# Kernel optimization log

Hardware: AMD Instinct MI355X
Metric: run time of the kernel (lower is better)

Reference implementation:

```python
import jax, jax.numpy as jnp
import numpy as np

N = 4096        # nodes
IN_FEATS = 256
N_HIDDEN = 128
N_CLASSES = 32
E = 131072      # edges for the GAE blocks (avg degree 32)
TEMP = 0.2
ALPHA = 1.0
EPS = 1e-6
CHUNK = 64      # row-chunk size for masked max aggregation


def _glorot(key, shape):
    fan = shape[0] + shape[1]
    return jax.random.normal(key, shape, jnp.float32) * jnp.sqrt(2.0 / fan)


def setup_inputs():
    key = jax.random.key(0)
    ks = jax.random.split(key, 20)
    return {
        'adj': jax.random.uniform(ks[0], (N, N), jnp.float32),
        'inputs': jax.random.normal(ks[1], (N, IN_FEATS), jnp.float32),
        'feat_inputs': jax.random.normal(ks[2], (N, IN_FEATS), jnp.float32),
        'u': jax.random.uniform(ks[3], (N, N), jnp.float32),
        'src': jax.random.randint(ks[4], (E,), 0, N, jnp.int32),
        'dst': jax.random.randint(ks[5], (E,), 0, N, jnp.int32),
        # GAE GraphConv params (in->hidden, hidden->hidden)
        'gc0_W': _glorot(ks[6], (IN_FEATS, N_HIDDEN)), 'gc0_b': jnp.zeros((N_HIDDEN,), jnp.float32),
        'gc1_W': _glorot(ks[7], (N_HIDDEN, N_HIDDEN)), 'gc1_b': jnp.zeros((N_HIDDEN,), jnp.float32),
        # GraphSAGE layer 0 (in -> hidden), maxpool aggregator
        'p0_W': _glorot(ks[8], (IN_FEATS, IN_FEATS)), 'p0_b': jnp.zeros((IN_FEATS,), jnp.float32),
        'l0_W': _glorot(ks[9], (IN_FEATS, N_HIDDEN)), 'l0_b': jnp.zeros((N_HIDDEN,), jnp.float32),
        'b0': jnp.zeros((N_HIDDEN,), jnp.float32),
        # GraphSAGE layer 1 (hidden -> hidden)
        'p1_W': _glorot(ks[10], (N_HIDDEN, N_HIDDEN)), 'p1_b': jnp.zeros((N_HIDDEN,), jnp.float32),
        'l1_W': _glorot(ks[11], (N_HIDDEN, N_HIDDEN)), 'l1_b': jnp.zeros((N_HIDDEN,), jnp.float32),
        'b1': jnp.zeros((N_HIDDEN,), jnp.float32),
        # GraphSAGE layer 2 (hidden -> classes)
        'p2_W': _glorot(ks[12], (N_HIDDEN, N_HIDDEN)), 'p2_b': jnp.zeros((N_HIDDEN,), jnp.float32),
        'l2_W': _glorot(ks[13], (N_HIDDEN, N_CLASSES)), 'l2_b': jnp.zeros((N_CLASSES,), jnp.float32),
        'b2': jnp.zeros((N_CLASSES,), jnp.float32),
    }


def _graph_conv(h, W, b, src, dst, out_norm, in_norm):
    # DGL GraphConv, norm='both': D_in^{-1/2} A D_out^{-1/2} X W + b
    h = h @ W
    h = h * out_norm[:, None]
    agg = jax.ops.segment_sum(h[src], dst, num_segments=N)
    return agg * in_norm[:, None] + b


def _masked_max(mask, z):
    # h_new[i] = max_{j: mask[i, j]} z[j]; chunk over destination rows to bound memory
    n, d = z.shape
    m = mask.reshape(n // CHUNK, CHUNK, n)
    def body(carry, mc):
        out = jnp.max(jnp.where(mc[:, :, None], z[None, :, :], -jnp.inf), axis=1)
        return carry, out
    _, outs = jax.lax.scan(body, None, m)
    return outs.reshape(n, d)


def _l2norm(x):
    return x / jnp.maximum(jnp.linalg.norm(x, axis=1, keepdims=True), 1e-12)


def _forward(adj, inputs, feat_inputs, u, src, dst,
             gc0_W, gc0_b, gc1_W, gc1_b,
             p0_W, p0_b, l0_W, l0_b, b0,
             p1_W, p1_b, l1_W, l1_b, b1,
             p2_W, p2_b, l2_W, l2_b, b2):
    ones = jnp.ones((E,), jnp.float32)
    out_norm = jnp.maximum(jax.ops.segment_sum(ones, src, num_segments=N), 1.0) ** -0.5
    in_norm = jnp.maximum(jax.ops.segment_sum(ones, dst, num_segments=N), 1.0) ** -0.5
    # --- GAE encode (dropout inactive at inference) ---
    h = jax.nn.relu(_graph_conv(inputs, gc0_W, gc0_b, src, dst, out_norm, in_norm))
    h = _graph_conv(h, gc1_W, gc1_b, src, dst, out_norm, in_norm)
    # --- GAE decode ---
    ep = jax.nn.sigmoid(h @ h.T)
    # --- interpolate ---
    P = ALPHA * (ep / jnp.max(ep)) + (1.0 - ALPHA) * adj
    # --- RelaxedBernoulli straight-through sampling ---
    Pc = jnp.clip(P, EPS, 1.0 - EPS)
    uc = jnp.clip(u, EPS, 1.0 - EPS)
    logits = jnp.log(Pc) - jnp.log1p(-Pc)
    noise = jnp.log(uc) - jnp.log1p(-uc)        # logistic noise
    soft = jax.nn.sigmoid((logits + noise) / TEMP)
    y = soft + jax.lax.stop_gradient(jnp.round(soft) - soft)
    yt = jnp.triu(y, 1)
    A = yt + yt.T
    # --- normalize_adj: diag=1, L1 row normalize; original detaches here ---
    eye = jnp.eye(N, dtype=bool)
    A = jnp.where(eye, 1.0, A)
    A = A / jnp.maximum(jnp.sum(A, axis=1, keepdims=True), 1e-12)
    A = jax.lax.stop_gradient(A)
    mask = A != 0.0   # symmetric graph structure incl. self-loops
    # --- GraphSAGE with maxpool aggregator (dropout inactive) ---
    h = feat_inputs
    layers = ((p0_W, p0_b, l0_W, l0_b, b0, False),
              (p1_W, p1_b, l1_W, l1_b, b1, False),
              (p2_W, p2_b, l2_W, l2_b, b2, True))
    for pW, pb, lW, lb, bb, last in layers:
        z = jax.nn.relu(h @ pW + pb)
        agg = _masked_max(mask, z)
        h = agg @ lW + lb + bb
        if not last:
            h = _l2norm(jax.nn.relu(h))
    return h


def reference(adj, inputs, feat_inputs, u, src, dst,
              gc0_W, gc0_b, gc1_W, gc1_b,
              p0_W, p0_b, l0_W, l0_b, b0,
              p1_W, p1_b, l1_W, l1_b, b1,
              p2_W, p2_b, l2_W, l2_b, b2):
    return _forward(adj, inputs, feat_inputs, u, src, dst,
                    gc0_W, gc0_b, gc1_W, gc1_b,
                    p0_W, p0_b, l0_W, l0_b, b0,
                    p1_W, p1_b, l1_W, l1_b, b1,
                    p2_W, p2_b, l2_W, l2_b, b2)
```

## Files before the change

kernel.cpp:

```cpp
#include <hip/hip_runtime.h>
#include <hip/hip_fp16.h>
#include <cstdint>
#include <cstddef>

#define NN 4096
#define EE 131072
#define TS 64

__device__ __forceinline__ unsigned fkey(float f) {
    unsigned u = __float_as_uint(f);
    return (u & 0x80000000u) ? ~u : (u | 0x80000000u);
}
__device__ __forceinline__ float funkey(unsigned k) {
    unsigned u = (k & 0x80000000u) ? (k & 0x7fffffffu) : ~k;
    return __uint_as_float(u);
}

__device__ __forceinline__ void pkmax(unsigned& a, unsigned x) {
    asm("v_pk_max_f16 %0, %0, %1" : "+v"(a) : "v"(x));
}
__device__ __forceinline__ unsigned bit_sext_s(unsigned w, int off) {
    return (unsigned)(((int)(w << (31 - off))) >> 31);
}

__global__ void k_count(const int* __restrict__ src, const int* __restrict__ dst,
                        int* __restrict__ cs, int* __restrict__ cd) {
    int e = blockIdx.x * 256 + threadIdx.x;
    if (e < EE) {
        atomicAdd(&cs[src[e]], 1);
        atomicAdd(&cd[dst[e]], 1);
    }
}

__global__ void k_norm(const int* __restrict__ cs, const int* __restrict__ cd,
                       float* __restrict__ on, float* __restrict__ inn) {
    int i = blockIdx.x * 256 + threadIdx.x;
    if (i < NN) {
        int a = cs[i] > 1 ? cs[i] : 1;
        int b = cd[i] > 1 ? cd[i] : 1;
        on[i]  = 1.0f / sqrtf((float)a);
        inn[i] = 1.0f / sqrtf((float)b);
    }
}

template<int K, int ND, int RB>
__global__ void k_gemm_scale(const float* __restrict__ X, const float* __restrict__ W,
                             const float* __restrict__ scale, float* __restrict__ out) {
    __shared__ float xr[RB][K];
    int i0 = blockIdx.x * RB;
    for (int t = threadIdx.x; t < RB * K; t += ND)
        xr[t / K][t % K] = X[(size_t)(i0 + t / K) * K + t % K];
    __syncthreads();
    int j = threadIdx.x;
    float acc[RB];
    #pragma unroll
    for (int r = 0; r < RB; ++r) acc[r] = 0.0f;
    #pragma unroll 4
    for (int k = 0; k < K; ++k) {
        float w = W[k * ND + j];
        #pragma unroll
        for (int r = 0; r < RB; ++r) acc[r] = fmaf(xr[r][k], w, acc[r]);
    }
    #pragma unroll
    for (int r = 0; r < RB; ++r)
        out[(size_t)(i0 + r) * ND + j] = acc[r] * scale[i0 + r];
}

template<int K, int ND, int RB, int H16>
__global__ void k_gemm_ab(const float* __restrict__ X, const float* __restrict__ W,
                          const float* __restrict__ b1, float* __restrict__ out) {
    __shared__ float xr[RB][K];
    int i0 = blockIdx.x * RB;
    for (int t = threadIdx.x; t < RB * K; t += ND)
        xr[t / K][t % K] = X[(size_t)(i0 + t / K) * K + t % K];
    __syncthreads();
    int j = threadIdx.x;
    float acc[RB];
    #pragma unroll
    for (int r = 0; r < RB; ++r) acc[r] = 0.0f;
    #pragma unroll 4
    for (int k = 0; k < K; ++k) {
        float w = W[k * ND + j];
        #pragma unroll
        for (int r = 0; r < RB; ++r) acc[r] = fmaf(xr[r][k], w, acc[r]);
    }
    if constexpr (H16) {
        unsigned* oh = (unsigned*)out;
        #pragma unroll
        for (int r = 0; r < RB; ++r) {
            float v = fmaxf(acc[r] + b1[j], 0.0f);
            float o2 = __shfl_xor(v, 1, 64);
            if ((j & 1) == 0) {
                __half2 h = __floats2half2_rn(v, o2);
                oh[(size_t)(i0 + r) * (ND / 2) + (j >> 1)] = *(unsigned*)&h;
            }
        }
    } else {
        #pragma unroll
        for (int r = 0; r < RB; ++r)
            out[(size_t)(i0 + r) * ND + j] = acc[r] + b1[j];
    }
}

template<int K, int ND, int NS, int RB, int L2N>
__global__ void k_gemm_mrgh(const unsigned* __restrict__ Xh, size_t xstride,
                            const float* __restrict__ W,
                            const float* __restrict__ b1, const float* __restrict__ b2,
                            float* __restrict__ out) {
    __shared__ float xr[RB][K];
    int i0 = blockIdx.x * RB;
    for (int t = threadIdx.x; t < RB * (K / 2); t += ND) {
        int r = t / (K / 2), c = t % (K / 2);
        size_t off = (size_t)(i0 + r) * (K / 2) + c;
        unsigned v = Xh[off];
        #pragma unroll
        for (int s = 1; s < NS; ++s) pkmax(v, Xh[(size_t)s * xstride + off]);
        __half2 h = *(__half2*)&v;
        float2 f = __half22float2(h);
        xr[r][2 * c] = f.x;
        xr[r][2 * c + 1] = f.y;
    }
    __syncthreads();
    int j = threadIdx.x;
    float acc[RB];
    #pragma unroll
    for (int r = 0; r < RB; ++r) acc[r] = 0.0f;
    #pragma unroll 4
    for (int k = 0; k < K; ++k) {
        float w = W[k * ND + j];
        #pragma unroll
        for (int r = 0; r < RB; ++r) acc[r] = fmaf(xr[r][k], w, acc[r]);
    }
    if constexpr (L2N) {
        float v[RB], ss[RB];
        #pragma unroll
        for (int r = 0; r < RB; ++r) {
            float t = acc[r] + b1[j];
            if (b2) t += b2[j];
            v[r] = fmaxf(t, 0.0f);
            ss[r] = v[r] * v[r];
        }
        #pragma unroll
        for (int o = 1; o < 64; o <<= 1)
            #pragma unroll
            for (int r = 0; r < RB; ++r) ss[r] += __shfl_xor(ss[r], o, 64);
        __shared__ float sred[RB][2];
        if ((threadIdx.x & 63) == 0)
            #pragma unroll
            for (int r = 0; r < RB; ++r) sred[r][threadIdx.x >> 6] = ss[r];
        __syncthreads();
        #pragma unroll
        for (int r = 0; r < RB; ++r) {
            float tot = sred[r][0] + sred[r][1];
            out[(size_t)(i0 + r) * ND + j] = v[r] / fmaxf(sqrtf(tot), 1e-12f);
        }
    } else {
        #pragma unroll
        for (int r = 0; r < RB; ++r) {
            float v = acc[r] + b1[j];
            if (b2) v += b2[j];
            out[(size_t)(i0 + r) * ND + j] = v;
        }
    }
}

__global__ void k_scatter(const float* __restrict__ t, const int* __restrict__ src,
                          const int* __restrict__ dst, float* __restrict__ agg) {
    int e = blockIdx.x;
    int j = threadIdx.x;
    int s = src[e], d = dst[e];
    atomicAdd(&agg[(size_t)d * 128 + j], t[(size_t)s * 128 + j]);
}

__global__ void k_gcn_out(const float* __restrict__ agg, const float* __restrict__ inn,
                          const float* __restrict__ b, float* __restrict__ out, int do_relu) {
    int idx = blockIdx.x * 256 + threadIdx.x;
    int i = idx >> 7, j = idx & 127;
    float v = agg[idx] * inn[i] + b[j];
    if (do_relu) v = fmaxf(v, 0.0f);
    out[idx] = v;
}

template<int MODE>
__global__ __launch_bounds__(256, 4) void k_stile(const float* __restrict__ h,
                                                  const float* __restrict__ u,
                                                  unsigned* __restrict__ smax_key,
                                                  unsigned* __restrict__ mb) {
    int ti = blockIdx.y, tj = blockIdx.x;
    if (tj < ti) return;
    __shared__ float Ah[TS][68];
    __shared__ float Bh[TS][68];
    int tid = threadIdx.x;
    int tx = tid & 15, ty = tid >> 4;
    const float* ha = h + (size_t)ti * TS * 128;
    const float* hb = h + (size_t)tj * TS * 128;

    float acc[4][4];
    #pragma unroll
    for (int r = 0; r < 4; ++r)
        #pragma unroll
        for (int c = 0; c < 4; ++c) acc[r][c] = 0.0f;

    for (int half = 0; half < 2; ++half) {
        __syncthreads();
        #pragma unroll
        for (int t = 0; t < 4; ++t) {
            int f = tid + t * 256;
            int row = f >> 4, kk = f & 15;
            *(float4*)&Ah[row][kk * 4] = *(const float4*)(ha + (size_t)row * 128 + half * 64 + kk * 4);
            *(float4*)&Bh[row][kk * 4] = *(const float4*)(hb + (size_t)row * 128 + half * 64 + kk * 4);
        }
        __syncthreads();
        #pragma unroll 2
        for (int k4 = 0; k4 < 16; ++k4) {
            float4 a[4], b[4];
            #pragma unroll
            for (int r = 0; r < 4; ++r) a[r] = *(const float4*)&Ah[ty + 16 * r][k4 * 4];
            #pragma unroll
            for (int c = 0; c < 4; ++c) b[c] = *(const float4*)&Bh[tx + 16 * c][k4 * 4];
            #pragma unroll
            for (int r = 0; r < 4; ++r)
                #pragma unroll
                for (int c = 0; c < 4; ++c) {
                    acc[r][c] = fmaf(a[r].x, b[c].x, acc[r][c]);
                    acc[r][c] = fmaf(a[r].y, b[c].y, acc[r][c]);
                    acc[r][c] = fmaf(a[r].z, b[c].z, acc[r][c]);
                    acc[r][c] = fmaf(a[r].w, b[c].w, acc[r][c]);
                }
        }
    }

    if constexpr (MODE == 0) {
        float m = -3.4e38f;
        #pragma unroll
        for (int r = 0; r < 4; ++r)
            #pragma unroll
            for (int c = 0; c < 4; ++c) m = fmaxf(m, acc[r][c]);
        #pragma unroll
        for (int o = 1; o < 64; o <<= 1) m = fmaxf(m, __shfl_xor(m, o, 64));
        __shared__ float wm[4];
        if ((tid & 63) == 0) wm[tid >> 6] = m;
        __syncthreads();
        if (tid == 0) {
            float mm = fmaxf(fmaxf(wm[0], wm[1]), fmaxf(wm[2], wm[3]));
            atomicMax(smax_key, fkey(mm));
        }
    } else {
        float smax = funkey(*smax_key);
        float epmax = 1.0f / (1.0f + expf(-smax));
        __shared__ unsigned lm[TS][2];
        __shared__ unsigned lmT[TS][2];
        if (tid < 128) { lm[tid >> 1][tid & 1] = 0u; lmT[tid >> 1][tid & 1] = 0u; }
        __syncthreads();
        #pragma unroll
        for (int r = 0; r < 4; ++r) {
            #pragma unroll
            for (int c = 0; c < 4; ++c) {
                int li = ty + 16 * r, lj = tx + 16 * c;
                int gi = ti * TS + li, gj = tj * TS + lj;
                bool bit = false;
                if (gi < gj) {
                    float ep = 1.0f / (1.0f + expf(-acc[r][c]));
                    float P = ep / epmax;
                    float Pc = fminf(fmaxf(P, 1e-6f), 1.0f - 1e-6f);
                    float uu = u[(size_t)gi * NN + gj];
                    float ucv = fminf(fmaxf(uu, 1e-6f), 1.0f - 1e-6f);
                    bit = Pc > (1.0f - ucv);
                } else if (gi == gj) {
                    bit = true;
                }
                if (bit) {
                    atomicOr(&lm[li][lj >> 5], 1u << (lj & 31));
                    atomicOr(&lmT[lj][li >> 5], 1u << (li & 31));
                }
            }
        }
        __syncthreads();
        if (tid < 128) {
            int r = tid >> 1, wq = tid & 1;
            unsigned word = lm[r][wq];
            if (ti == tj) word |= lmT[r][wq];
            mb[(size_t)(ti * TS + r) * 128 + tj * 2 + wq] = word;
        } else if (ti != tj) {
            int r = (tid - 128) >> 1, wq = tid & 1;
            mb[(size_t)(tj * TS + r) * 128 + ti * 2 + wq] = lmT[r][wq];
        }
    }
}

__global__ __launch_bounds__(256, 4) void k_stile_store(const float* __restrict__ h,
                                                        float* __restrict__ S,
                                                        unsigned* __restrict__ smax_key) {
    int ti = blockIdx.y, tj = blockIdx.x;
    if (tj < ti) return;
    __shared__ float Ah[TS][68];
    __shared__ float Bh[TS][68];
    int tid = threadIdx.x;
    int tx = tid & 15, ty = tid >> 4;
    const float* ha = h + (size_t)ti * TS * 128;
    const float* hb = h + (size_t)tj * TS * 128;

    float acc[4][4];
    #pragma unroll
    for (int r = 0; r < 4; ++r)
        #pragma unroll
        for (int c = 0; c < 4; ++c) acc[r][c] = 0.0f;

    for (int half = 0; half < 2; ++half) {
        __syncthreads();
        #pragma unroll
        for (int t = 0; t < 4; ++t) {
            int f = tid + t * 256;
            int row = f >> 4, kk = f & 15;
            *(float4*)&Ah[row][kk * 4] = *(const float4*)(ha + (size_t)row * 128 + half * 64 + kk * 4);
            *(float4*)&Bh[row][kk * 4] = *(const float4*)(hb + (size_t)row * 128 + half * 64 + kk * 4);
        }
        __syncthreads();
        #pragma unroll 2
        for (int k4 = 0; k4 < 16; ++k4) {
            float4 a[4], b[4];
            #pragma unroll
            for (int r = 0; r < 4; ++r) a[r] = *(const float4*)&Ah[ty + 16 * r][k4 * 4];
            #pragma unroll
            for (int c = 0; c < 4; ++c) b[c] = *(const float4*)&Bh[tx + 16 * c][k4 * 4];
            #pragma unroll
            for (int r = 0; r < 4; ++r)
                #pragma unroll
                for (int c = 0; c < 4; ++c) {
                    acc[r][c] = fmaf(a[r].x, b[c].x, acc[r][c]);
                    acc[r][c] = fmaf(a[r].y, b[c].y, acc[r][c]);
                    acc[r][c] = fmaf(a[r].z, b[c].z, acc[r][c]);
                    acc[r][c] = fmaf(a[r].w, b[c].w, acc[r][c]);
                }
        }
    }

    float* sp = S + (size_t)(ti * 64 + tj) * 4096;
    #pragma unroll
    for (int r = 0; r < 4; ++r)
        #pragma unroll
        for (int c = 0; c < 4; ++c)
            sp[(ty + 16 * r) * 64 + tx + 16 * c] = acc[r][c];

    float m = -3.4e38f;
    #pragma unroll
    for (int r = 0; r < 4; ++r)
        #pragma unroll
        for (int c = 0; c < 4; ++c) m = fmaxf(m, acc[r][c]);
    #pragma unroll
    for (int o = 1; o < 64; o <<= 1) m = fmaxf(m, __shfl_xor(m, o, 64));
    __shared__ float wm[4];
    if ((tid & 63) == 0) wm[tid >> 6] = m;
    __syncthreads();
    if (tid == 0)
        atomicMax(smax_key, fkey(fmaxf(fmaxf(wm[0], wm[1]), fmaxf(wm[2], wm[3]))));
}

__global__ __launch_bounds__(256, 4) void k_bitemit(const float* __restrict__ S,
                                                    const float* __restrict__ u,
                                                    const unsigned* __restrict__ smax_key,
                                                    unsigned* __restrict__ mb) {
    int ti = blockIdx.y, tj = blockIdx.x;
    if (tj < ti) return;
    int tid = threadIdx.x;
    int tx = tid & 15, ty = tid >> 4;
    float smax = funkey(*smax_key);
    float epmax = 1.0f / (1.0f + expf(-smax));
    __shared__ unsigned lm[TS][2];
    __shared__ unsigned lmT[TS][2];
    if (tid < 128) { lm[tid >> 1][tid & 1] = 0u; lmT[tid >> 1][tid & 1] = 0u; }
    __syncthreads();
    const float* sp = S + (size_t)(ti * 64 + tj) * 4096;
    #pragma unroll
    for (int r = 0; r < 4; ++r) {
        #pragma unroll
        for (int c = 0; c < 4; ++c) {
            int li = ty + 16 * r, lj = tx + 16 * c;
            int gi = ti * TS + li, gj = tj * TS + lj;
            bool bit = false;
            if (gi < gj) {
                float ep = 1.0f / (1.0f + expf(-sp[li * 64 + lj]));
                float P = ep / epmax;
                float Pc = fminf(fmaxf(P, 1e-6f), 1.0f - 1e-6f);
                float uu = u[(size_t)gi * NN + gj];
                float ucv = fminf(fmaxf(uu, 1e-6f), 1.0f - 1e-6f);
                bit = Pc > (1.0f - ucv);
            } else if (gi == gj) {
                bit = true;
            }
            if (bit) {
                atomicOr(&lm[li][lj >> 5], 1u << (lj & 31));
                atomicOr(&lmT[lj][li >> 5], 1u << (li & 31));
            }
        }
    }
    __syncthreads();
    if (tid < 128) {
        int r = tid >> 1, wq = tid & 1;
        unsigned word = lm[r][wq];
        if (ti == tj) word |= lmT[r][wq];
        mb[(size_t)(ti * TS + r) * 128 + tj * 2 + wq] = word;
    } else if (ti != tj) {
        int r = (tid - 128) >> 1, wq = tid & 1;
        mb[(size_t)(tj * TS + r) * 128 + ti * 2 + wq] = lmT[r][wq];
    }
}

template<int RT, int JS>
__global__ __launch_bounds__(256, 8) void k_mmax256h(const unsigned* __restrict__ mb,
                                                     const unsigned* __restrict__ zh,
                                                     unsigned* __restrict__ pmh) {
    constexpr int JPS = NN / JS;
    constexpr int WPS = JPS / 32;
    constexpr int RPG = RT / 4;
    constexpr int NRB = NN / RT;
    int rowblk = blockIdx.x % NRB, js = blockIdx.x / NRB;
    int i0 = rowblk * RT;

    __shared__ unsigned msk[RT][WPS + 1];
    {
        int t = threadIdx.x;
        msk[t / WPS][t % WPS] = mb[(size_t)(i0 + t / WPS) * 128 + js * WPS + t % WPS];
    }
    __syncthreads();

    int d = threadIdx.x & 63;
    int g = threadIdx.x >> 6;
    const uint2* zbase = (const uint2*)zh + (size_t)js * JPS * 64 + d;

    uint2 acc[RPG];
    #pragma unroll
    for (int r = 0; r < RPG; ++r) acc[r] = make_uint2(0u, 0u);

    #pragma unroll 1
    for (int wq = 0; wq < WPS; ++wq) {
        unsigned m[RPG];
        #pragma unroll
        for (int r = 0; r < RPG; ++r)
            m[r] = (unsigned)__builtin_amdgcn_readfirstlane((int)msk[g * RPG + r][wq]);
        const uint2* zp = zbase + (size_t)(wq * 32) * 64;
        #pragma unroll 2
        for (int j4 = 0; j4 < 32; j4 += 4) {
            uint2 z0 = zp[0 * 64];
            uint2 z1 = zp[1 * 64];
            uint2 z2 = zp[2 * 64];
            uint2 z3 = zp[3 * 64];
            #pragma unroll
            for (int r = 0; r < RPG; ++r) {
                unsigned s0 = bit_sext_s(m[r], j4 + 0);
                unsigned s1 = bit_sext_s(m[r], j4 + 1);
                unsigned s2 = bit_sext_s(m[r], j4 + 2);
                unsigned s3 = bit_sext_s(m[r], j4 + 3);
                pkmax(acc[r].x, s0 & z0.x); pkmax(acc[r].y, s0 & z0.y);
                pkmax(acc[r].x, s1 & z1.x); pkmax(acc[r].y, s1 & z1.y);
                pkmax(acc[r].x, s2 & z2.x); pkmax(acc[r].y, s2 & z2.y);
                pkmax(acc[r].x, s3 & z3.x); pkmax(acc[r].y, s3 & z3.y);
            }
            zp += 4 * 64;
        }
    }

    uint2* po = (uint2*)(pmh + (size_t)js * NN * 128);
    #pragma unroll
    for (int r = 0; r < RPG; ++r)
        po[(size_t)(i0 + g * RPG + r) * 64 + d] = acc[r];
}

template<int RT, int JS>
__global__ __launch_bounds__(256, 8) void k_mmax128h(const unsigned* __restrict__ mb,
                                                     const unsigned* __restrict__ zh,
                                                     unsigned* __restrict__ pmh) {
    constexpr int JPS = NN / JS;
    constexpr int WPS = JPS / 32;
    constexpr int RPG = RT / 4;
    constexpr int NRB = NN / RT;
    int rowblk = blockIdx.x % NRB, js = blockIdx.x / NRB;
    int i0 = rowblk * RT;

    __shared__ unsigned msk[RT][WPS + 1];
    {
        int t = threadIdx.x;
        msk[t / WPS][t % WPS] = mb[(size_t)(i0 + t / WPS) * 128 + js * WPS + t % WPS];
    }
    __syncthreads();

    int lane = threadIdx.x & 63;
    int g = threadIdx.x >> 6;
    unsigned jpar = lane >> 5;
    int d2 = lane & 31;
    const uint2* zbase = (const uint2*)zh + (size_t)js * JPS * 32 + d2;

    uint2 acc[RPG];
    #pragma unroll
    for (int r = 0; r < RPG; ++r) acc[r] = make_uint2(0u, 0u);

    #pragma unroll 1
    for (int wq = 0; wq < WPS; ++wq) {
        unsigned m[RPG];
        #pragma unroll
        for (int r = 0; r < RPG; ++r)
            m[r] = (unsigned)__builtin_amdgcn_readfirstlane((int)msk[g * RPG + r][wq]);
        const uint2* zp = zbase + (size_t)(wq * 32) * 32;
        #pragma unroll 2
        for (int j4 = 0; j4 < 32; j4 += 4) {
            uint2 za = zp[(size_t)jpar * 32];
            uint2 zb = zp[(size_t)(2 + jpar) * 32];
            int oa = j4 + (int)jpar, ob = j4 + 2 + (int)jpar;
            #pragma unroll
            for (int r = 0; r < RPG; ++r) {
                unsigned sa = bit_sext_s(m[r], oa);
                unsigned sb = bit_sext_s(m[r], ob);
                pkmax(acc[r].x, sa & za.x); pkmax(acc[r].y, sa & za.y);
                pkmax(acc[r].x, sb & zb.x); pkmax(acc[r].y, sb & zb.y);
            }
            zp += 4 * 32;
        }
    }

    #pragma unroll
    for (int r = 0; r < RPG; ++r) {
        unsigned ox = __shfl_xor(acc[r].x, 32, 64);
        unsigned oy = __shfl_xor(acc[r].y, 32, 64);
        pkmax(acc[r].x, ox);
        pkmax(acc[r].y, oy);
    }
    if (!jpar) {
        uint2* po = (uint2*)(pmh + (size_t)js * NN * 64);
        #pragma unroll
        for (int r = 0; r < RPG; ++r)
            po[(size_t)(i0 + g * RPG + r) * 32 + d2] = acc[r];
    }
}

template<int NS>
__global__ void k_gemm_final(const unsigned* __restrict__ Xh, size_t xstride,
                             const float* __restrict__ W,
                             const float* __restrict__ b1, const float* __restrict__ b2,
                             float* __restrict__ out) {
    __shared__ float xr[4][128];
    int i0 = blockIdx.x * 4;
    for (int t = threadIdx.x; t < 256; t += 128) {
        int r = t >> 6, c = t & 63;
        size_t off = (size_t)(i0 + r) * 64 + c;
        unsigned v = Xh[off];
        #pragma unroll
        for (int s = 1; s < NS; ++s) pkmax(v, Xh[(size_t)s * xstride + off]);
        __half2 h = *(__half2*)&v;
        float2 f = __half22float2(h);
        xr[r][2 * c] = f.x;
        xr[r][2 * c + 1] = f.y;
    }
    __syncthreads();
    int il = threadIdx.x >> 5, j = threadIdx.x & 31;
    float acc = 0.0f;
    #pragma unroll 8
    for (int k = 0; k < 128; ++k) acc = fmaf(xr[il][k], W[k * 32 + j], acc);
    out[(size_t)(i0 + il) * 32 + j] = acc + b1[j] + b2[j];
}

extern "C" void kernel_launch(void* const* d_in, const int* in_sizes, int n_in,
                              void* d_out, int out_size, void* d_ws, size_t ws_size,
                              hipStream_t stream) {
    const float* inputs = (const float*)d_in[1];
    const float* feat   = (const float*)d_in[2];
    const float* u      = (const float*)d_in[3];
    const int*   src    = (const int*)d_in[4];
    const int*   dst    = (const int*)d_in[5];
    const float* gc0W = (const float*)d_in[6],  *gc0b = (const float*)d_in[7];
    const float* gc1W = (const float*)d_in[8],  *gc1b = (const float*)d_in[9];
    const float* p0W  = (const float*)d_in[10], *p0b  = (const float*)d_in[11];
    const float* l0W  = (const float*)d_in[12], *l0b  = (const float*)d_in[13];
    const float* b0   = (const float*)d_in[14];
    const float* p1W  = (const float*)d_in[15], *p1b  = (const float*)d_in[16];
    const float* l1W  = (const float*)d_in[17], *l1b  = (const float*)d_in[18];
    const float* b1   = (const float*)d_in[19];
    const float* p2W  = (const float*)d_in[20], *p2b  = (const float*)d_in[21];
    const float* l2W  = (const float*)d_in[22], *l2b  = (const float*)d_in[23];
    const float* b2   = (const float*)d_in[24];
    float* out = (float*)d_out;

    const size_t MB = 1048576;
    char* w = (char*)d_ws;
    int*      cnt_src  = (int*)(w + 0);
    int*      cnt_dst  = (int*)(w + 16384);
    float*    on       = (float*)(w + 32768);
    float*    inn      = (float*)(w + 49152);
    unsigned* smax_key = (unsigned*)(w + 65536);
    char*     big      = w + 131072;
    float*    tmp      = (float*)(big);
    float*    agg      = (float*)(big + 2 * MB);
    float*    hbuf     = (float*)(big + 4 * MB);
    unsigned* mb       = (unsigned*)(big + 6 * MB);
    unsigned* zh       = (unsigned*)(big + 8 * MB);
    unsigned* pmh      = (unsigned*)(big + 12 * MB);
    float*    hs       = (float*)(big + 44 * MB);
    float*    Sbuf     = (float*)(big + 46 * MB);
    bool use_sstore = ws_size >= 131072 + 110 * MB;

    hipMemsetAsync(w, 0, 131072, stream);
    k_count<<<EE / 256, 256, 0, stream>>>(src, dst, cnt_src, cnt_dst);
    k_norm<<<NN / 256, 256, 0, stream>>>(cnt_src, cnt_dst, on, inn);

    k_gemm_scale<256, 128, 4><<<NN / 4, 128, 0, stream>>>(inputs, gc0W, on, tmp);
    hipMemsetAsync(agg, 0, (size_t)NN * 128 * 4, stream);
    k_scatter<<<EE, 128, 0, stream>>>(tmp, src, dst, agg);
    k_gcn_out<<<NN * 128 / 256, 256, 0, stream>>>(agg, inn, gc0b, hbuf, 1);

    k_gemm_scale<128, 128, 4><<<NN / 4, 128, 0, stream>>>(hbuf, gc1W, on, tmp);
    hipMemsetAsync(agg, 0, (size_t)NN * 128 * 4, stream);
    k_scatter<<<EE, 128, 0, stream>>>(tmp, src, dst, agg);
    k_gcn_out<<<NN * 128 / 256, 256, 0, stream>>>(agg, inn, gc1b, hbuf, 0);

    dim3 tg(64, 64);
    if (use_sstore) {
        k_stile_store<<<tg, 256, 0, stream>>>(hbuf, Sbuf, smax_key);
        k_bitemit<<<tg, 256, 0, stream>>>(Sbuf, u, smax_key, mb);
    } else {
        k_stile<0><<<tg, 256, 0, stream>>>(hbuf, nullptr, smax_key, nullptr);
        k_stile<1><<<tg, 256, 0, stream>>>(hbuf, u, smax_key, mb);
    }

    k_gemm_ab<256, 256, 4, 1><<<NN / 4, 256, 0, stream>>>(feat, p0W, p0b, (float*)zh);
    k_mmax256h<16, 8><<<(NN / 16) * 8, 256, 0, stream>>>(mb, zh, pmh);
    k_gemm_mrgh<256, 128, 8, 4, 1><<<NN / 4, 128, 0, stream>>>(pmh, (size_t)NN * 128, l0W, l0b, b0, hs);

    k_gemm_ab<128, 128, 4, 1><<<NN / 4, 128, 0, stream>>>(hs, p1W, p1b, (float*)zh);
    k_mmax128h<16, 8><<<(NN / 16) * 8, 256, 0, stream>>>(mb, zh, pmh);
    k_gemm_mrgh<128, 128, 8, 4, 1><<<NN / 4, 128, 0, stream>>>(pmh, (size_t)NN * 64, l1W, l1b, b1, tmp);

    k_gemm_ab<128, 128, 4, 1><<<NN / 4, 128, 0, stream>>>(tmp, p2W, p2b, (float*)zh);
    k_mmax128h<16, 8><<<(NN / 16) * 8, 256, 0, stream>>>(mb, zh, pmh);
    k_gemm_final<8><<<NN / 4, 128, 0, stream>>>(pmh, (size_t)NN * 64, l2W, l2b, b2, out);
}
```

Baseline: 670.3 us.

## Replace atomic edge scatter with CSR bucketing and per-node gather

Builds a CSR-style incoming-edge list per destination node (prefix sum over in-degree counts plus bucketing) once. Both GCN aggregation layers then gather source rows per destination, with the normalisation, bias and relu fused in. This removes the 131072-block float atomicAdd scatter, the memsets of the aggregation buffer and the separate output kernel. In exchange it adds a single-block prefix-sum kernel and a bucketing pass. Summation order is no longer the atomic order and now depends on bucket order, which is nondeterministic.

```diff
diff --git a/kernel.cpp b/kernel.cpp
--- a/kernel.cpp
+++ b/kernel.cpp
@@ -41,6 +41,59 @@
         on[i]  = 1.0f / sqrtf((float)a);
         inn[i] = 1.0f / sqrtf((float)b);
     }
+}
+
+__global__ void k_prefix(const int* __restrict__ cnt, int* __restrict__ off) {
+    __shared__ int ls[1024];
+    int t = threadIdx.x;
+    int base[4];
+    int s = 0;
+    #pragma unroll
+    for (int k = 0; k < 4; ++k) { base[k] = s; s += cnt[t * 4 + k]; }
+    ls[t] = s;
+    __syncthreads();
+    for (int o = 1; o < 1024; o <<= 1) {
+        int v = (t >= o) ? ls[t - o] : 0;
+        __syncthreads();
+        ls[t] += v;
+        __syncthreads();
+    }
+    int excl = (t == 0) ? 0 : ls[t - 1];
+    #pragma unroll
+    for (int k = 0; k < 4; ++k) off[t * 4 + k] = excl + base[k];
+    if (t == 1023) off[4096] = ls[1023];
+}
+
+__global__ void k_bucket(const int* __restrict__ src, const int* __restrict__ dst,
+                         const int* __restrict__ off, int* __restrict__ cursor,
+                         int* __restrict__ elist) {
+    int e = blockIdx.x * 256 + threadIdx.x;
+    if (e < EE) {
+        int d = dst[e];
+        int pos = atomicAdd(&cursor[d], 1);
+        elist[off[d] + pos] = src[e];
+    }
+}
+
+__global__ void k_gather(const float* __restrict__ t, const int* __restrict__ elist,
+                         const int* __restrict__ off, const float* __restrict__ inn,
+                         const float* __restrict__ b, float* __restrict__ outp,
+                         int do_relu) {
+    int d = blockIdx.x;
+    int j = threadIdx.x;
+    int s0 = off[d], s1 = off[d + 1];
+    float a0 = 0.f, a1 = 0.f, a2 = 0.f, a3 = 0.f;
+    int e = s0;
+    for (; e + 4 <= s1; e += 4) {
+        a0 += t[(size_t)elist[e + 0] * 128 + j];
+        a1 += t[(size_t)elist[e + 1] * 128 + j];
+        a2 += t[(size_t)elist[e + 2] * 128 + j];
+        a3 += t[(size_t)elist[e + 3] * 128 + j];
+    }
+    for (; e < s1; ++e) a0 += t[(size_t)elist[e] * 128 + j];
+    float v = ((a0 + a1) + (a2 + a3)) * inn[d] + b[j];
+    if (do_relu) v = fmaxf(v, 0.0f);
+    outp[(size_t)d * 128 + j] = v;
 }
 
 template<int K, int ND, int RB>
@@ -162,23 +215,6 @@
             out[(size_t)(i0 + r) * ND + j] = v;
         }
     }
-}
-
-__global__ void k_scatter(const float* __restrict__ t, const int* __restrict__ src,
-                          const int* __restrict__ dst, float* __restrict__ agg) {
-    int e = blockIdx.x;
-    int j = threadIdx.x;
-    int s = src[e], d = dst[e];
-    atomicAdd(&agg[(size_t)d * 128 + j], t[(size_t)s * 128 + j]);
-}
-
-__global__ void k_gcn_out(const float* __restrict__ agg, const float* __restrict__ inn,
-                          const float* __restrict__ b, float* __restrict__ out, int do_relu) {
-    int idx = blockIdx.x * 256 + threadIdx.x;
-    int i = idx >> 7, j = idx & 127;
-    float v = agg[idx] * inn[i] + b[j];
-    if (do_relu) v = fmaxf(v, 0.0f);
-    out[idx] = v;
 }
 
 template<int MODE>
@@ -586,9 +622,11 @@
     float*    on       = (float*)(w + 32768);
     float*    inn      = (float*)(w + 49152);
     unsigned* smax_key = (unsigned*)(w + 65536);
+    int*      cursor   = (int*)(w + 81920);
+    int*      eoff     = (int*)(w + 98304);
     char*     big      = w + 131072;
     float*    tmp      = (float*)(big);
-    float*    agg      = (float*)(big + 2 * MB);
+    int*      elist    = (int*)(big + 2 * MB);
     float*    hbuf     = (float*)(big + 4 * MB);
     unsigned* mb       = (unsigned*)(big + 6 * MB);
     unsigned* zh       = (unsigned*)(big + 8 * MB);
@@ -600,16 +638,14 @@
     hipMemsetAsync(w, 0, 131072, stream);
     k_count<<<EE / 256, 256, 0, stream>>>(src, dst, cnt_src, cnt_dst);
     k_norm<<<NN / 256, 256, 0, stream>>>(cnt_src, cnt_dst, on, inn);
+    k_prefix<<<1, 1024, 0, stream>>>(cnt_dst, eoff);
+    k_bucket<<<EE / 256, 256, 0, stream>>>(src, dst, eoff, cursor, elist);
 
     k_gemm_scale<256, 128, 4><<<NN / 4, 128, 0, stream>>>(inputs, gc0W, on, tmp);
-    hipMemsetAsync(agg, 0, (size_t)NN * 128 * 4, stream);
-    k_scatter<<<EE, 128, 0, stream>>>(tmp, src, dst, agg);
-    k_gcn_out<<<NN * 128 / 256, 256, 0, stream>>>(agg, inn, gc0b, hbuf, 1);
+    k_gather<<<NN, 128, 0, stream>>>(tmp, elist, eoff, inn, gc0b, hbuf, 1);
 
     k_gemm_scale<128, 128, 4><<<NN / 4, 128, 0, stream>>>(hbuf, gc1W, on, tmp);
-    hipMemsetAsync(agg, 0, (size_t)NN * 128 * 4, stream);
-    k_scatter<<<EE, 128, 0, stream>>>(tmp, src, dst, agg);
-    k_gcn_out<<<NN * 128 / 256, 256, 0, stream>>>(agg, inn, gc1b, hbuf, 0);
+    k_gather<<<NN, 128, 0, stream>>>(tmp, elist, eoff, inn, gc1b, hbuf, 0);
 
     dim3 tg(64, 64);
     if (use_sstore) {
```

Result: faster. 576.8 us (-13.9%).
